# Kernel optimization log

Measured on AMD Instinct MI355X. Metric: run time of the kernel, lower is better.

The kernel has to match this reference:

```python
import jax, jax.numpy as jnp
import numpy as np

HIDDEN = 1024
N_HEADS = 16
HEAD_DIM = 64
LOCAL_WINDOW = 1024
GLOBAL_STRIDE = 512


def _sparse_mask(seq_len):
    # local sliding window (half-window each side), strided global columns, causal
    i = jnp.arange(seq_len)[:, None]
    j = jnp.arange(seq_len)[None, :]
    diff = i - j
    local = jnp.abs(diff) <= (LOCAL_WINDOW // 2)
    glob = (j % GLOBAL_STRIDE) == 0
    causal = diff >= 0
    return (local | glob) & causal  # [S, S] bool


def setup_inputs() -> dict:
    key = jax.random.key(0)
    k0, k1, k2, k3, k4 = jax.random.split(key, 5)
    B, S = 1, 2048
    scale = 1.0 / np.sqrt(HIDDEN)
    return {
        "hidden_states": jax.random.normal(k0, (B, S, HIDDEN), dtype=jnp.float32),
        "w_q": jax.random.normal(k1, (HIDDEN, N_HEADS * HEAD_DIM), dtype=jnp.float32) * scale,
        "w_k": jax.random.normal(k2, (HIDDEN, N_HEADS * HEAD_DIM), dtype=jnp.float32) * scale,
        "w_v": jax.random.normal(k3, (HIDDEN, N_HEADS * HEAD_DIM), dtype=jnp.float32) * scale,
        "w_o": jax.random.normal(k4, (N_HEADS * HEAD_DIM, HIDDEN), dtype=jnp.float32) * scale,
    }


def reference(hidden_states, w_q, w_k, w_v, w_o):
    B, S, _ = hidden_states.shape

    def shape(x):  # [B,S,H*D] -> [B,H,S,D]
        return x.reshape(B, S, N_HEADS, HEAD_DIM).transpose(0, 2, 1, 3)

    q = shape(hidden_states @ w_q)
    k = shape(hidden_states @ w_k)
    v = shape(hidden_states @ w_v)

    scores = jnp.einsum("bhqd,bhkd->bhqk", q, k) / np.sqrt(HEAD_DIM)
    mask = _sparse_mask(S)  # [S,S]
    scores = jnp.where(mask[None, None], scores, -jnp.inf)
    attn = jax.nn.softmax(scores, axis=-1)
    out = jnp.einsum("bhqk,bhkd->bhqd", attn, v)
    out = out.transpose(0, 2, 1, 3).reshape(B, S, N_HEADS * HEAD_DIM)
    return out @ w_o
```

## Files before the change

### kernel.cpp

```cpp
#include <hip/hip_runtime.h>

#define SEQ 2048
#define HID 1024
#define NH 16
#define HD 64
#define QKVLD 3072

typedef __attribute__((ext_vector_type(8))) short bf16x8;
typedef __attribute__((ext_vector_type(4))) float f32x4;

__device__ __forceinline__ unsigned short f2bf(float f) {
  unsigned int x = __float_as_uint(f);
  x += 0x7fffu + ((x >> 16) & 1u);
  return (unsigned short)(x >> 16);
}

__device__ __forceinline__ float bf2f(unsigned short u) {
  return __uint_as_float(((unsigned int)u) << 16);
}

__device__ __forceinline__ void gld_lds16(const void* g, void* l) {
  __builtin_amdgcn_global_load_lds((__attribute__((address_space(1))) void*)g,
                                   (__attribute__((address_space(3))) void*)l, 16, 0, 0);
}

__global__ void prep(const float* __restrict__ X, const float* __restrict__ Wq,
                     const float* __restrict__ Wk, const float* __restrict__ Wv,
                     const float* __restrict__ Wo, unsigned short* __restrict__ Xb,
                     unsigned short* __restrict__ WtQKV, unsigned short* __restrict__ WtO) {
  const int z = blockIdx.z;
  if (z == 4) {
    int bid = blockIdx.y * 32 + blockIdx.x;
    int t = threadIdx.y * 32 + threadIdx.x;
    size_t base = (size_t)bid * 2048 + t * 4;
#pragma unroll
    for (int half = 0; half < 2; half++) {
      float4 v = *(const float4*)(X + base + half * 1024);
      ushort4 o;
      o.x = f2bf(v.x); o.y = f2bf(v.y); o.z = f2bf(v.z); o.w = f2bf(v.w);
      *(ushort4*)(Xb + base + half * 1024) = o;
    }
    return;
  }
  __shared__ float tile[32][33];
  const float* S = (z == 0) ? Wq : (z == 1) ? Wk : (z == 2) ? Wv : Wo;
  unsigned short* D = (z < 3) ? (WtQKV + (size_t)z * HID * HID) : WtO;
  const float scale = (z == 0) ? 0.125f : 1.0f;
  int r0 = blockIdx.y * 32, c0 = blockIdx.x * 32;
  int tx = threadIdx.x, ty = threadIdx.y;
#pragma unroll
  for (int k = 0; k < 4; k++)
    tile[ty + k * 8][tx] = S[(size_t)(r0 + ty + k * 8) * HID + c0 + tx];
  __syncthreads();
#pragma unroll
  for (int k = 0; k < 4; k++)
    D[(size_t)(c0 + ty + k * 8) * HID + r0 + tx] = f2bf(scale * tile[tx][ty + k * 8]);
}

template <int BN, int OUT>
__global__ __launch_bounds__(256, 2) void gemm_bt(const unsigned short* __restrict__ A,
                                                  const unsigned short* __restrict__ Bt,
                                                  void* __restrict__ Cout,
                                                  unsigned short* __restrict__ Vout,
                                                  int M, int N, int K) {
  constexpr int NI = BN / 32;
  __shared__ unsigned short As[128 * 64];
  __shared__ unsigned short Bs[BN * 64];
  const int tid = threadIdx.x;
  const int lane = tid & 63;
  const int w = tid >> 6;
  const int wm = w >> 1, wn = w & 1;
  const int quad = lane >> 4, l16 = lane & 15;
  const int bm = blockIdx.y * 128, bn = blockIdx.x * BN;

  f32x4 acc[4][NI] = {};

  for (int k0 = 0; k0 < K; k0 += 64) {
#pragma unroll
    for (int c = tid; c < 128 * 8; c += 256) {
      int r = c >> 3, kc = c & 7;
      int g = (kc & 4) + ((kc & 3) ^ (r & 3));
      gld_lds16(A + (size_t)(bm + r) * K + k0 + g * 8, As + c * 8);
    }
#pragma unroll
    for (int c = tid; c < BN * 8; c += 256) {
      int r = c >> 3, kc = c & 7;
      int g = (kc & 4) + ((kc & 3) ^ (r & 3));
      gld_lds16(Bt + (size_t)(bn + r) * K + k0 + g * 8, Bs + c * 8);
    }
    __syncthreads();
    bf16x8 af[2][4], bfr[2][NI];
#pragma unroll
    for (int ks = 0; ks < 2; ks++) {
#pragma unroll
      for (int mi = 0; mi < 4; mi++) {
        int m = wm * 64 + mi * 16 + l16;
        af[ks][mi] = *(const bf16x8*)(As + (m * 8 + ks * 4 + (quad ^ (m & 3))) * 8);
      }
#pragma unroll
      for (int ni = 0; ni < NI; ni++) {
        int n = wn * (BN / 2) + ni * 16 + l16;
        bfr[ks][ni] = *(const bf16x8*)(Bs + (n * 8 + ks * 4 + (quad ^ (n & 3))) * 8);
      }
    }
#pragma unroll
    for (int mi = 0; mi < 4; mi++)
#pragma unroll
      for (int ni = 0; ni < NI; ni++) {
        acc[mi][ni] = __builtin_amdgcn_mfma_f32_16x16x32_bf16(af[0][mi], bfr[0][ni], acc[mi][ni], 0, 0, 0);
        acc[mi][ni] = __builtin_amdgcn_mfma_f32_16x16x32_bf16(af[1][mi], bfr[1][ni], acc[mi][ni], 0, 0, 0);
      }
    __syncthreads();
  }

#pragma unroll
  for (int mi = 0; mi < 4; mi++) {
#pragma unroll
    for (int ni = 0; ni < NI; ni++) {
      int row = bm + wm * 64 + mi * 16 + quad * 4;
      int col = bn + wn * (BN / 2) + ni * 16 + l16;
      if (OUT == 0) {
#pragma unroll
        for (int r = 0; r < 4; r++)
          ((float*)Cout)[(size_t)(row + r) * N + col] = acc[mi][ni][r];
      } else {
        if (col < 2 * HID) {
#pragma unroll
          for (int r = 0; r < 4; r++)
            ((unsigned short*)Cout)[(size_t)(row + r) * N + col] = f2bf(acc[mi][ni][r]);
        } else {
          ushort4 o;
          o.x = f2bf(acc[mi][ni][0]); o.y = f2bf(acc[mi][ni][1]);
          o.z = f2bf(acc[mi][ni][2]); o.w = f2bf(acc[mi][ni][3]);
          *(ushort4*)(Vout + (size_t)(col - 2 * HID) * SEQ + row) = o;
        }
      }
    }
  }
}

__global__ __launch_bounds__(256, 2) void attn_sparse(const unsigned short* __restrict__ QKV,
                                                      const unsigned short* __restrict__ VtG,
                                                      unsigned short* __restrict__ AttO) {
  __shared__ unsigned short Ks[64 * 64];
  __shared__ unsigned short Vt[64 * 64];
  __shared__ unsigned short Pw[4][16 * 72];
  const int h = blockIdx.y;
  const int qbase = blockIdx.x * 64;
  const int tid = threadIdx.x;
  const int lane = tid & 63, w = tid >> 6;
  const int quad = lane >> 4, l16 = lane & 15;
  const int qrow0 = qbase + w * 16;
  unsigned short* pws = &Pw[w][0];

  bf16x8 aq[2];
  {
    const unsigned short* qp = QKV + (size_t)(qrow0 + l16) * QKVLD + h * HD + quad * 8;
    aq[0] = *(const bf16x8*)qp;
    aq[1] = *(const bf16x8*)(qp + 32);
  }

  f32x4 accO[4] = {};
  float lsum = 0.f;

  const int jlo = (qbase >= 512) ? (qbase - 512) : 0;
  const int ng = (jlo > 0) ? ((jlo + 511) >> 9) : 0;
  const int ntl = ((qbase - jlo) >> 6) + 1;

  for (int t = 0; t < ntl; t++) {
    const int j0 = jlo + t * 64;
    if (t > 0) __syncthreads();
#pragma unroll
    for (int c = tid; c < 512; c += 256) {
      int r = c >> 3, kc = c & 7;
      int g = (kc & 4) + ((kc & 3) ^ (r & 3));
      gld_lds16(QKV + (size_t)(j0 + r) * QKVLD + HID + h * HD + g * 8, Ks + c * 8);
      gld_lds16(VtG + (size_t)(h * HD + r) * SEQ + j0 + g * 8, Vt + c * 8);
    }
    __syncthreads();

    f32x4 s[4] = {};
#pragma unroll
    for (int nj = 0; nj < 4; nj++) {
      int row = nj * 16 + l16;
#pragma unroll
      for (int ks = 0; ks < 2; ks++) {
        bf16x8 ak = *(const bf16x8*)(Ks + (row * 8 + ks * 4 + (quad ^ (row & 3))) * 8);
        s[nj] = __builtin_amdgcn_mfma_f32_16x16x32_bf16(ak, aq[ks], s[nj], 0, 0, 0);
      }
    }

    const bool isdiag = (t == ntl - 1);
    const bool istrail = (t == 0) && (qbase >= 512);
    const int trailg = (istrail && ((j0 & 511) == 0)) ? 1 : 0;
    const int db = qrow0 + l16 - j0 - quad * 4;
#pragma unroll
    for (int nj = 0; nj < 4; nj++) {
      float p[4];
#pragma unroll
      for (int r = 0; r < 4; r++) {
        float x = fminf(s[nj][r], 60.0f);
        int d = db - nj * 16 - r;
        bool valid = true;
        if (isdiag) valid = (d >= 0);
        else if (istrail) valid = (d <= 512) || (trailg && (nj * 16 + quad * 4 + r) == 0);
        x = valid ? x : -1e30f;
        p[r] = __expf(x);
        lsum += p[r];
      }
      unsigned int u01 = (unsigned)f2bf(p[0]) | ((unsigned)f2bf(p[1]) << 16);
      unsigned int u23 = (unsigned)f2bf(p[2]) | ((unsigned)f2bf(p[3]) << 16);
      *(uint2*)(pws + l16 * 72 + nj * 16 + quad * 4) = make_uint2(u01, u23);
    }

#pragma unroll
    for (int kk = 0; kk < 2; kk++) {
      bf16x8 bp = *(const bf16x8*)(pws + l16 * 72 + kk * 32 + quad * 8);
#pragma unroll
      for (int nd = 0; nd < 4; nd++) {
        int row = nd * 16 + l16;
        bf16x8 av = *(const bf16x8*)(Vt + (row * 8 + kk * 4 + (quad ^ (row & 3))) * 8);
        accO[nd] = __builtin_amdgcn_mfma_f32_16x16x32_bf16(av, bp, accO[nd], 0, 0, 0);
      }
    }
  }

  if (ng > 0) {
    __syncthreads();
    if (tid < ng * 8) {
      int r = tid >> 3, kc = tid & 7;
      int g = (kc & 4) + ((kc & 3) ^ (r & 3));
      *(uint4*)(Ks + tid * 8) =
          *(const uint4*)(QKV + ((size_t)r << 9) * QKVLD + HID + h * HD + g * 8);
    }
    if (tid < ng * 64) {
      int d = tid & 63, c = tid >> 6;
      Vt[(d * 8 + (d & 3)) * 8 + c] = VtG[(size_t)(h * HD + d) * SEQ + ((size_t)c << 9)];
    }
    __syncthreads();
    f32x4 s0 = {};
#pragma unroll
    for (int ks = 0; ks < 2; ks++) {
      bf16x8 ak = *(const bf16x8*)(Ks + (l16 * 8 + ks * 4 + (quad ^ (l16 & 3))) * 8);
      s0 = __builtin_amdgcn_mfma_f32_16x16x32_bf16(ak, aq[ks], s0, 0, 0, 0);
    }
    float p[4];
#pragma unroll
    for (int r = 0; r < 4; r++) {
      p[r] = ((quad * 4 + r) < ng) ? __expf(fminf(s0[r], 60.0f)) : 0.f;
      lsum += p[r];
    }
    unsigned int u01 = (unsigned)f2bf(p[0]) | ((unsigned)f2bf(p[1]) << 16);
    unsigned int u23 = (unsigned)f2bf(p[2]) | ((unsigned)f2bf(p[3]) << 16);
    *(uint2*)(pws + l16 * 72 + quad * 4) = make_uint2(u01, u23);
    *(uint2*)(pws + l16 * 72 + 16 + quad * 4) = make_uint2(0, 0);
    bf16x8 bp = *(const bf16x8*)(pws + l16 * 72 + quad * 8);
#pragma unroll
    for (int nd = 0; nd < 4; nd++) {
      int row = nd * 16 + l16;
      bf16x8 av = *(const bf16x8*)(Vt + (row * 8 + (quad ^ (row & 3))) * 8);
      accO[nd] = __builtin_amdgcn_mfma_f32_16x16x32_bf16(av, bp, accO[nd], 0, 0, 0);
    }
  }

  lsum += __shfl_xor(lsum, 16);
  lsum += __shfl_xor(lsum, 32);
  const float rl = 1.0f / lsum;
  const int i = qrow0 + l16;
#pragma unroll
  for (int nd = 0; nd < 4; nd++) {
    ushort4 o;
    o.x = f2bf(accO[nd][0] * rl);
    o.y = f2bf(accO[nd][1] * rl);
    o.z = f2bf(accO[nd][2] * rl);
    o.w = f2bf(accO[nd][3] * rl);
    *(ushort4*)(AttO + (size_t)i * HID + h * HD + nd * 16 + quad * 4) = o;
  }
}

extern "C" void kernel_launch(void* const* d_in, const int* in_sizes, int n_in,
                              void* d_out, int out_size, void* d_ws, size_t ws_size,
                              hipStream_t stream) {
  const float* X  = (const float*)d_in[0];
  const float* Wq = (const float*)d_in[1];
  const float* Wk = (const float*)d_in[2];
  const float* Wv = (const float*)d_in[3];
  const float* Wo = (const float*)d_in[4];
  float* out = (float*)d_out;

  unsigned short* Xb    = (unsigned short*)d_ws;
  unsigned short* WtQKV = Xb + (size_t)SEQ * HID;
  unsigned short* WtO   = WtQKV + (size_t)QKVLD * HID;
  unsigned short* QKV   = WtO + (size_t)HID * HID;
  unsigned short* VtG   = QKV + (size_t)SEQ * QKVLD;
  unsigned short* AttO  = VtG + (size_t)HID * SEQ;

  prep<<<dim3(32, 32, 5), dim3(32, 8), 0, stream>>>(X, Wq, Wk, Wv, Wo, Xb, WtQKV, WtO);

  gemm_bt<96, 2><<<dim3(QKVLD / 96, SEQ / 128), dim3(256), 0, stream>>>(
      Xb, WtQKV, QKV, VtG, SEQ, QKVLD, HID);

  attn_sparse<<<dim3(SEQ / 64, NH), dim3(256), 0, stream>>>(QKV, VtG, AttO);

  gemm_bt<64, 0><<<dim3(HID / 64, SEQ / 128), dim3(256), 0, stream>>>(
      AttO, WtO, out, nullptr, SEQ, HID, HID);
}
```

Measured before the change: 133.1 us.

## Fuse all stages into one persistent kernel with grid barriers and XCD-aware tiling

Replaces the four separate launches (prep, QKV GEMM, sparse attention, output GEMM) with one persistent 512-block kernel. Stages are separated by software grid barriers built on atomics. Block-to-tile mappings are remapped by XCD index to improve L2 locality. The output GEMM uses 64x64 tiles, bf16 packing uses the hardware paired conversion, and the fminf clamp before exp is removed. This trades launch gaps and stage tails for barrier spin cost and a risk of deadlock if all 512 blocks are not co-resident.

```diff
diff --git a/kernel.cpp b/kernel.cpp
--- a/kernel.cpp
+++ b/kernel.cpp
@@ -1,4 +1,5 @@
 #include <hip/hip_runtime.h>
+#include <hip/hip_bf16.h>
 
 #define SEQ 2048
 #define HID 1024
@@ -8,15 +9,18 @@
 
 typedef __attribute__((ext_vector_type(8))) short bf16x8;
 typedef __attribute__((ext_vector_type(4))) float f32x4;
-
-__device__ __forceinline__ unsigned short f2bf(float f) {
+typedef unsigned short us;
+
+__device__ __forceinline__ us f2bf(float f) {
   unsigned int x = __float_as_uint(f);
   x += 0x7fffu + ((x >> 16) & 1u);
-  return (unsigned short)(x >> 16);
-}
-
-__device__ __forceinline__ float bf2f(unsigned short u) {
-  return __uint_as_float(((unsigned int)u) << 16);
+  return (us)(x >> 16);
+}
+
+__device__ __forceinline__ unsigned int pkbf(float a, float b) {
+  union { __hip_bfloat162 h2; unsigned int u; } cvt;
+  cvt.h2 = __float22bfloat162_rn(make_float2(a, b));
+  return cvt.u;
 }
 
 __device__ __forceinline__ void gld_lds16(const void* g, void* l) {
@@ -24,257 +28,323 @@
                                    (__attribute__((address_space(3))) void*)l, 16, 0, 0);
 }
 
-__global__ void prep(const float* __restrict__ X, const float* __restrict__ Wq,
-                     const float* __restrict__ Wk, const float* __restrict__ Wv,
-                     const float* __restrict__ Wo, unsigned short* __restrict__ Xb,
-                     unsigned short* __restrict__ WtQKV, unsigned short* __restrict__ WtO) {
-  const int z = blockIdx.z;
-  if (z == 4) {
-    int bid = blockIdx.y * 32 + blockIdx.x;
-    int t = threadIdx.y * 32 + threadIdx.x;
-    size_t base = (size_t)bid * 2048 + t * 4;
-#pragma unroll
-    for (int half = 0; half < 2; half++) {
-      float4 v = *(const float4*)(X + base + half * 1024);
-      ushort4 o;
-      o.x = f2bf(v.x); o.y = f2bf(v.y); o.z = f2bf(v.z); o.w = f2bf(v.w);
-      *(ushort4*)(Xb + base + half * 1024) = o;
-    }
-    return;
-  }
-  __shared__ float tile[32][33];
-  const float* S = (z == 0) ? Wq : (z == 1) ? Wk : (z == 2) ? Wv : Wo;
-  unsigned short* D = (z < 3) ? (WtQKV + (size_t)z * HID * HID) : WtO;
-  const float scale = (z == 0) ? 0.125f : 1.0f;
-  int r0 = blockIdx.y * 32, c0 = blockIdx.x * 32;
-  int tx = threadIdx.x, ty = threadIdx.y;
-#pragma unroll
-  for (int k = 0; k < 4; k++)
-    tile[ty + k * 8][tx] = S[(size_t)(r0 + ty + k * 8) * HID + c0 + tx];
+__device__ __forceinline__ f32x4 mfma(bf16x8 a, bf16x8 b, f32x4 c) {
+  return __builtin_amdgcn_mfma_f32_16x16x32_bf16(a, b, c, 0, 0, 0);
+}
+
+#define NBLK 512
+
+__device__ __forceinline__ void gridbar(unsigned int* bar, int idx) {
   __syncthreads();
-#pragma unroll
-  for (int k = 0; k < 4; k++)
-    D[(size_t)(c0 + ty + k * 8) * HID + r0 + tx] = f2bf(scale * tile[tx][ty + k * 8]);
-}
-
-template <int BN, int OUT>
-__global__ __launch_bounds__(256, 2) void gemm_bt(const unsigned short* __restrict__ A,
-                                                  const unsigned short* __restrict__ Bt,
-                                                  void* __restrict__ Cout,
-                                                  unsigned short* __restrict__ Vout,
-                                                  int M, int N, int K) {
-  constexpr int NI = BN / 32;
-  __shared__ unsigned short As[128 * 64];
-  __shared__ unsigned short Bs[BN * 64];
-  const int tid = threadIdx.x;
-  const int lane = tid & 63;
-  const int w = tid >> 6;
-  const int wm = w >> 1, wn = w & 1;
-  const int quad = lane >> 4, l16 = lane & 15;
-  const int bm = blockIdx.y * 128, bn = blockIdx.x * BN;
-
-  f32x4 acc[4][NI] = {};
-
-  for (int k0 = 0; k0 < K; k0 += 64) {
-#pragma unroll
-    for (int c = tid; c < 128 * 8; c += 256) {
-      int r = c >> 3, kc = c & 7;
-      int g = (kc & 4) + ((kc & 3) ^ (r & 3));
-      gld_lds16(A + (size_t)(bm + r) * K + k0 + g * 8, As + c * 8);
-    }
-#pragma unroll
-    for (int c = tid; c < BN * 8; c += 256) {
-      int r = c >> 3, kc = c & 7;
-      int g = (kc & 4) + ((kc & 3) ^ (r & 3));
-      gld_lds16(Bt + (size_t)(bn + r) * K + k0 + g * 8, Bs + c * 8);
-    }
-    __syncthreads();
-    bf16x8 af[2][4], bfr[2][NI];
-#pragma unroll
-    for (int ks = 0; ks < 2; ks++) {
-#pragma unroll
-      for (int mi = 0; mi < 4; mi++) {
-        int m = wm * 64 + mi * 16 + l16;
-        af[ks][mi] = *(const bf16x8*)(As + (m * 8 + ks * 4 + (quad ^ (m & 3))) * 8);
-      }
-#pragma unroll
-      for (int ni = 0; ni < NI; ni++) {
-        int n = wn * (BN / 2) + ni * 16 + l16;
-        bfr[ks][ni] = *(const bf16x8*)(Bs + (n * 8 + ks * 4 + (quad ^ (n & 3))) * 8);
-      }
-    }
-#pragma unroll
-    for (int mi = 0; mi < 4; mi++)
-#pragma unroll
-      for (int ni = 0; ni < NI; ni++) {
-        acc[mi][ni] = __builtin_amdgcn_mfma_f32_16x16x32_bf16(af[0][mi], bfr[0][ni], acc[mi][ni], 0, 0, 0);
-        acc[mi][ni] = __builtin_amdgcn_mfma_f32_16x16x32_bf16(af[1][mi], bfr[1][ni], acc[mi][ni], 0, 0, 0);
-      }
-    __syncthreads();
-  }
-
-#pragma unroll
-  for (int mi = 0; mi < 4; mi++) {
-#pragma unroll
-    for (int ni = 0; ni < NI; ni++) {
-      int row = bm + wm * 64 + mi * 16 + quad * 4;
-      int col = bn + wn * (BN / 2) + ni * 16 + l16;
-      if (OUT == 0) {
-#pragma unroll
-        for (int r = 0; r < 4; r++)
-          ((float*)Cout)[(size_t)(row + r) * N + col] = acc[mi][ni][r];
-      } else {
-        if (col < 2 * HID) {
-#pragma unroll
-          for (int r = 0; r < 4; r++)
-            ((unsigned short*)Cout)[(size_t)(row + r) * N + col] = f2bf(acc[mi][ni][r]);
-        } else {
-          ushort4 o;
-          o.x = f2bf(acc[mi][ni][0]); o.y = f2bf(acc[mi][ni][1]);
-          o.z = f2bf(acc[mi][ni][2]); o.w = f2bf(acc[mi][ni][3]);
-          *(ushort4*)(Vout + (size_t)(col - 2 * HID) * SEQ + row) = o;
-        }
-      }
-    }
-  }
-}
-
-__global__ __launch_bounds__(256, 2) void attn_sparse(const unsigned short* __restrict__ QKV,
-                                                      const unsigned short* __restrict__ VtG,
-                                                      unsigned short* __restrict__ AttO) {
-  __shared__ unsigned short Ks[64 * 64];
-  __shared__ unsigned short Vt[64 * 64];
-  __shared__ unsigned short Pw[4][16 * 72];
-  const int h = blockIdx.y;
-  const int qbase = blockIdx.x * 64;
+  if (threadIdx.x == 0) {
+    __threadfence();
+    unsigned int prev = atomicAdd(&bar[idx * 2], 1u);
+    if (prev == NBLK - 1) {
+      atomicExch(&bar[idx * 2 + 1], 1u);
+    } else {
+      while (atomicAdd(&bar[idx * 2 + 1], 0u) == 0u)
+        __builtin_amdgcn_s_sleep(8);
+    }
+    __threadfence();
+  }
+  __syncthreads();
+}
+
+__global__ void bar_init(unsigned int* bar) {
+  if (threadIdx.x < 8) bar[threadIdx.x] = 0u;
+}
+
+__global__ __launch_bounds__(256, 2) void fused(
+    const float* __restrict__ X, const float* __restrict__ Wq,
+    const float* __restrict__ Wk, const float* __restrict__ Wv,
+    const float* __restrict__ Wo, float* __restrict__ out,
+    us* __restrict__ Xb, us* __restrict__ WtQKV, us* __restrict__ WtO,
+    us* __restrict__ QKV, us* __restrict__ VtG, us* __restrict__ AttO,
+    unsigned int* bar) {
+  __shared__ __align__(16) unsigned char smem[28672];
+  const int lin = blockIdx.x;
   const int tid = threadIdx.x;
   const int lane = tid & 63, w = tid >> 6;
   const int quad = lane >> 4, l16 = lane & 15;
-  const int qrow0 = qbase + w * 16;
-  unsigned short* pws = &Pw[w][0];
-
-  bf16x8 aq[2];
+
   {
-    const unsigned short* qp = QKV + (size_t)(qrow0 + l16) * QKVLD + h * HD + quad * 8;
-    aq[0] = *(const bf16x8*)qp;
-    aq[1] = *(const bf16x8*)(qp + 32);
-  }
-
-  f32x4 accO[4] = {};
-  float lsum = 0.f;
-
-  const int jlo = (qbase >= 512) ? (qbase - 512) : 0;
-  const int ng = (jlo > 0) ? ((jlo + 511) >> 9) : 0;
-  const int ntl = ((qbase - jlo) >> 6) + 1;
-
-  for (int t = 0; t < ntl; t++) {
-    const int j0 = jlo + t * 64;
-    if (t > 0) __syncthreads();
-#pragma unroll
-    for (int c = tid; c < 512; c += 256) {
-      int r = c >> 3, kc = c & 7;
-      int g = (kc & 4) + ((kc & 3) ^ (r & 3));
-      gld_lds16(QKV + (size_t)(j0 + r) * QKVLD + HID + h * HD + g * 8, Ks + c * 8);
-      gld_lds16(VtG + (size_t)(h * HD + r) * SEQ + j0 + g * 8, Vt + c * 8);
-    }
-    __syncthreads();
-
-    f32x4 s[4] = {};
-#pragma unroll
-    for (int nj = 0; nj < 4; nj++) {
-      int row = nj * 16 + l16;
+    size_t base = (size_t)lin * 4096 + tid * 4;
+#pragma unroll
+    for (int i = 0; i < 4; i++) {
+      float4 v = *(const float4*)(X + base + i * 1024);
+      *(uint2*)(Xb + base + i * 1024) = make_uint2(pkbf(v.x, v.y), pkbf(v.z, v.w));
+    }
+    float* tile = (float*)smem;
+    const int tx = tid & 31, ty = tid >> 5;
+    for (int tt = lin; tt < 4096; tt += 512) {
+      const int z = tt >> 10, rem = tt & 1023;
+      const int r0 = (rem >> 5) * 32, c0 = (rem & 31) * 32;
+      const float* S = (z == 0) ? Wq : (z == 1) ? Wk : (z == 2) ? Wv : Wo;
+      us* D = (z < 3) ? (WtQKV + (size_t)z * HID * HID) : WtO;
+      const float scale = (z == 0) ? 0.125f : 1.0f;
+#pragma unroll
+      for (int k = 0; k < 4; k++)
+        tile[(ty + k * 8) * 33 + tx] = S[(size_t)(r0 + ty + k * 8) * HID + c0 + tx];
+      __syncthreads();
+#pragma unroll
+      for (int k = 0; k < 4; k++)
+        D[(size_t)(c0 + ty + k * 8) * HID + r0 + tx] = f2bf(scale * tile[tx * 33 + ty + k * 8]);
+      __syncthreads();
+    }
+  }
+  gridbar(bar, 0);
+
+  {
+    us* As = (us*)smem;
+    us* Bs = As + 128 * 64;
+    const int wm = w >> 1, wn = w & 1;
+    const int xcd = lin & 7, idx = lin >> 3;
+    const int bx = (xcd & 3) * 8 + (idx & 7);
+    const int by = (xcd >> 2) * 8 + (idx >> 3);
+    const int bm = by * 128, bn = bx * 96;
+
+    f32x4 acc[4][3] = {};
+
+    for (int k0 = 0; k0 < HID; k0 += 64) {
+#pragma unroll
+      for (int c = tid; c < 1024; c += 256) {
+        int r = c >> 3, kc = c & 7;
+        int g = (kc & 4) + ((kc & 3) ^ (r & 3));
+        gld_lds16(Xb + (size_t)(bm + r) * HID + k0 + g * 8, As + c * 8);
+      }
+#pragma unroll
+      for (int c = tid; c < 768; c += 256) {
+        int r = c >> 3, kc = c & 7;
+        int g = (kc & 4) + ((kc & 3) ^ (r & 3));
+        gld_lds16(WtQKV + (size_t)(bn + r) * HID + k0 + g * 8, Bs + c * 8);
+      }
+      __syncthreads();
+      bf16x8 af[2][4], bfr[2][3];
 #pragma unroll
       for (int ks = 0; ks < 2; ks++) {
-        bf16x8 ak = *(const bf16x8*)(Ks + (row * 8 + ks * 4 + (quad ^ (row & 3))) * 8);
-        s[nj] = __builtin_amdgcn_mfma_f32_16x16x32_bf16(ak, aq[ks], s[nj], 0, 0, 0);
-      }
-    }
-
-    const bool isdiag = (t == ntl - 1);
-    const bool istrail = (t == 0) && (qbase >= 512);
-    const int trailg = (istrail && ((j0 & 511) == 0)) ? 1 : 0;
-    const int db = qrow0 + l16 - j0 - quad * 4;
-#pragma unroll
-    for (int nj = 0; nj < 4; nj++) {
+#pragma unroll
+        for (int mi = 0; mi < 4; mi++) {
+          int m = wm * 64 + mi * 16 + l16;
+          af[ks][mi] = *(const bf16x8*)(As + (m * 8 + ks * 4 + (quad ^ (m & 3))) * 8);
+        }
+#pragma unroll
+        for (int ni = 0; ni < 3; ni++) {
+          int n = wn * 48 + ni * 16 + l16;
+          bfr[ks][ni] = *(const bf16x8*)(Bs + (n * 8 + ks * 4 + (quad ^ (n & 3))) * 8);
+        }
+      }
+#pragma unroll
+      for (int mi = 0; mi < 4; mi++)
+#pragma unroll
+        for (int ni = 0; ni < 3; ni++) {
+          acc[mi][ni] = mfma(af[0][mi], bfr[0][ni], acc[mi][ni]);
+          acc[mi][ni] = mfma(af[1][mi], bfr[1][ni], acc[mi][ni]);
+        }
+      __syncthreads();
+    }
+
+#pragma unroll
+    for (int mi = 0; mi < 4; mi++) {
+#pragma unroll
+      for (int ni = 0; ni < 3; ni++) {
+        int row = bm + wm * 64 + mi * 16 + quad * 4;
+        int col = bn + wn * 48 + ni * 16 + l16;
+        if (col < 2 * HID) {
+#pragma unroll
+          for (int r = 0; r < 4; r++)
+            QKV[(size_t)(row + r) * QKVLD + col] = f2bf(acc[mi][ni][r]);
+        } else {
+          *(uint2*)(VtG + (size_t)(col - 2 * HID) * SEQ + row) =
+              make_uint2(pkbf(acc[mi][ni][0], acc[mi][ni][1]),
+                         pkbf(acc[mi][ni][2], acc[mi][ni][3]));
+        }
+      }
+    }
+  }
+  gridbar(bar, 1);
+
+  {
+    us* Ks = (us*)smem;
+    us* Vt = Ks + 4096;
+    us* Pw = Vt + 4096;
+    const int xcd = lin & 7, slot = lin >> 3;
+    const int h = slot >> 2;
+    const int qbase = (xcd * 4 + (slot & 3)) * 64;
+    const int qrow0 = qbase + w * 16;
+    us* pws = Pw + w * (16 * 72);
+
+    bf16x8 aq[2];
+    {
+      const us* qp = QKV + (size_t)(qrow0 + l16) * QKVLD + h * HD + quad * 8;
+      aq[0] = *(const bf16x8*)qp;
+      aq[1] = *(const bf16x8*)(qp + 32);
+    }
+
+    f32x4 accO[4] = {};
+    float lsum = 0.f;
+
+    const int jlo = (qbase >= 512) ? (qbase - 512) : 0;
+    const int ng = (jlo > 0) ? ((jlo + 511) >> 9) : 0;
+    const int ntl = ((qbase - jlo) >> 6) + 1;
+
+    for (int t = 0; t < ntl; t++) {
+      const int j0 = jlo + t * 64;
+      if (t > 0) __syncthreads();
+#pragma unroll
+      for (int c = tid; c < 512; c += 256) {
+        int r = c >> 3, kc = c & 7;
+        int g = (kc & 4) + ((kc & 3) ^ (r & 3));
+        gld_lds16(QKV + (size_t)(j0 + r) * QKVLD + HID + h * HD + g * 8, Ks + c * 8);
+        gld_lds16(VtG + (size_t)(h * HD + r) * SEQ + j0 + g * 8, Vt + c * 8);
+      }
+      __syncthreads();
+
+      f32x4 s[4] = {};
+#pragma unroll
+      for (int nj = 0; nj < 4; nj++) {
+        int row = nj * 16 + l16;
+#pragma unroll
+        for (int ks = 0; ks < 2; ks++) {
+          bf16x8 ak = *(const bf16x8*)(Ks + (row * 8 + ks * 4 + (quad ^ (row & 3))) * 8);
+          s[nj] = mfma(ak, aq[ks], s[nj]);
+        }
+      }
+
+      const bool isdiag = (t == ntl - 1);
+      const bool istrail = (t == 0) && (qbase >= 512);
+      const int trailg = (istrail && ((j0 & 511) == 0)) ? 1 : 0;
+      const int db = qrow0 + l16 - j0 - quad * 4;
+#pragma unroll
+      for (int nj = 0; nj < 4; nj++) {
+        float p[4];
+#pragma unroll
+        for (int r = 0; r < 4; r++) {
+          float x = s[nj][r];
+          int d = db - nj * 16 - r;
+          bool valid = true;
+          if (isdiag) valid = (d >= 0);
+          else if (istrail) valid = (d <= 512) || (trailg && (nj * 16 + quad * 4 + r) == 0);
+          x = valid ? x : -1e30f;
+          p[r] = __expf(x);
+          lsum += p[r];
+        }
+        *(uint2*)(pws + l16 * 72 + nj * 16 + quad * 4) =
+            make_uint2(pkbf(p[0], p[1]), pkbf(p[2], p[3]));
+      }
+
+#pragma unroll
+      for (int kk = 0; kk < 2; kk++) {
+        bf16x8 bp = *(const bf16x8*)(pws + l16 * 72 + kk * 32 + quad * 8);
+#pragma unroll
+        for (int nd = 0; nd < 4; nd++) {
+          int row = nd * 16 + l16;
+          bf16x8 av = *(const bf16x8*)(Vt + (row * 8 + kk * 4 + (quad ^ (row & 3))) * 8);
+          accO[nd] = mfma(av, bp, accO[nd]);
+        }
+      }
+    }
+
+    if (ng > 0) {
+      __syncthreads();
+      if (tid < ng * 8) {
+        int r = tid >> 3, kc = tid & 7;
+        int g = (kc & 4) + ((kc & 3) ^ (r & 3));
+        *(uint4*)(Ks + tid * 8) =
+            *(const uint4*)(QKV + ((size_t)r << 9) * QKVLD + HID + h * HD + g * 8);
+      }
+      if (tid < ng * 64) {
+        int d = tid & 63, c = tid >> 6;
+        Vt[(d * 8 + (d & 3)) * 8 + c] = VtG[(size_t)(h * HD + d) * SEQ + ((size_t)c << 9)];
+      }
+      __syncthreads();
+      f32x4 s0 = {};
+#pragma unroll
+      for (int ks = 0; ks < 2; ks++) {
+        bf16x8 ak = *(const bf16x8*)(Ks + (l16 * 8 + ks * 4 + (quad ^ (l16 & 3))) * 8);
+        s0 = mfma(ak, aq[ks], s0);
+      }
       float p[4];
 #pragma unroll
       for (int r = 0; r < 4; r++) {
-        float x = fminf(s[nj][r], 60.0f);
-        int d = db - nj * 16 - r;
-        bool valid = true;
-        if (isdiag) valid = (d >= 0);
-        else if (istrail) valid = (d <= 512) || (trailg && (nj * 16 + quad * 4 + r) == 0);
-        x = valid ? x : -1e30f;
-        p[r] = __expf(x);
+        p[r] = ((quad * 4 + r) < ng) ? __expf(s0[r]) : 0.f;
         lsum += p[r];
       }
-      unsigned int u01 = (unsigned)f2bf(p[0]) | ((unsigned)f2bf(p[1]) << 16);
-      unsigned int u23 = (unsigned)f2bf(p[2]) | ((unsigned)f2bf(p[3]) << 16);
-      *(uint2*)(pws + l16 * 72 + nj * 16 + quad * 4) = make_uint2(u01, u23);
-    }
-
-#pragma unroll
-    for (int kk = 0; kk < 2; kk++) {
-      bf16x8 bp = *(const bf16x8*)(pws + l16 * 72 + kk * 32 + quad * 8);
+      *(uint2*)(pws + l16 * 72 + quad * 4) = make_uint2(pkbf(p[0], p[1]), pkbf(p[2], p[3]));
+      *(uint2*)(pws + l16 * 72 + 16 + quad * 4) = make_uint2(0, 0);
+      bf16x8 bp = *(const bf16x8*)(pws + l16 * 72 + quad * 8);
 #pragma unroll
       for (int nd = 0; nd < 4; nd++) {
         int row = nd * 16 + l16;
-        bf16x8 av = *(const bf16x8*)(Vt + (row * 8 + kk * 4 + (quad ^ (row & 3))) * 8);
-        accO[nd] = __builtin_amdgcn_mfma_f32_16x16x32_bf16(av, bp, accO[nd], 0, 0, 0);
-      }
-    }
-  }
-
-  if (ng > 0) {
-    __syncthreads();
-    if (tid < ng * 8) {
-      int r = tid >> 3, kc = tid & 7;
-      int g = (kc & 4) + ((kc & 3) ^ (r & 3));
-      *(uint4*)(Ks + tid * 8) =
-          *(const uint4*)(QKV + ((size_t)r << 9) * QKVLD + HID + h * HD + g * 8);
-    }
-    if (tid < ng * 64) {
-      int d = tid & 63, c = tid >> 6;
-      Vt[(d * 8 + (d & 3)) * 8 + c] = VtG[(size_t)(h * HD + d) * SEQ + ((size_t)c << 9)];
-    }
-    __syncthreads();
-    f32x4 s0 = {};
-#pragma unroll
-    for (int ks = 0; ks < 2; ks++) {
-      bf16x8 ak = *(const bf16x8*)(Ks + (l16 * 8 + ks * 4 + (quad ^ (l16 & 3))) * 8);
-      s0 = __builtin_amdgcn_mfma_f32_16x16x32_bf16(ak, aq[ks], s0, 0, 0, 0);
-    }
-    float p[4];
-#pragma unroll
-    for (int r = 0; r < 4; r++) {
-      p[r] = ((quad * 4 + r) < ng) ? __expf(fminf(s0[r], 60.0f)) : 0.f;
-      lsum += p[r];
-    }
-    unsigned int u01 = (unsigned)f2bf(p[0]) | ((unsigned)f2bf(p[1]) << 16);
-    unsigned int u23 = (unsigned)f2bf(p[2]) | ((unsigned)f2bf(p[3]) << 16);
-    *(uint2*)(pws + l16 * 72 + quad * 4) = make_uint2(u01, u23);
-    *(uint2*)(pws + l16 * 72 + 16 + quad * 4) = make_uint2(0, 0);
-    bf16x8 bp = *(const bf16x8*)(pws + l16 * 72 + quad * 8);
+        bf16x8 av = *(const bf16x8*)(Vt + (row * 8 + (quad ^ (row & 3))) * 8);
+        accO[nd] = mfma(av, bp, accO[nd]);
+      }
+    }
+
+    lsum += __shfl_xor(lsum, 16);
+    lsum += __shfl_xor(lsum, 32);
+    const float rl = 1.0f / lsum;
+    const int i = qrow0 + l16;
 #pragma unroll
     for (int nd = 0; nd < 4; nd++) {
-      int row = nd * 16 + l16;
-      bf16x8 av = *(const bf16x8*)(Vt + (row * 8 + (quad ^ (row & 3))) * 8);
-      accO[nd] = __builtin_amdgcn_mfma_f32_16x16x32_bf16(av, bp, accO[nd], 0, 0, 0);
-    }
-  }
-
-  lsum += __shfl_xor(lsum, 16);
-  lsum += __shfl_xor(lsum, 32);
-  const float rl = 1.0f / lsum;
-  const int i = qrow0 + l16;
-#pragma unroll
-  for (int nd = 0; nd < 4; nd++) {
-    ushort4 o;
-    o.x = f2bf(accO[nd][0] * rl);
-    o.y = f2bf(accO[nd][1] * rl);
-    o.z = f2bf(accO[nd][2] * rl);
-    o.w = f2bf(accO[nd][3] * rl);
-    *(ushort4*)(AttO + (size_t)i * HID + h * HD + nd * 16 + quad * 4) = o;
+      *(uint2*)(AttO + (size_t)i * HID + h * HD + nd * 16 + quad * 4) =
+          make_uint2(pkbf(accO[nd][0] * rl, accO[nd][1] * rl),
+                     pkbf(accO[nd][2] * rl, accO[nd][3] * rl));
+    }
+  }
+  gridbar(bar, 2);
+
+  {
+    us* As = (us*)smem;
+    us* Bs = As + 64 * 64;
+    const int wm = w >> 1, wn = w & 1;
+    const int xcd = lin & 7, idx = lin >> 3;
+    const int bx = (xcd & 3) * 4 + (idx & 3);
+    const int by = (xcd >> 2) * 16 + (idx >> 2);
+    const int bm = by * 64, bn = bx * 64;
+
+    f32x4 acc[2][2] = {};
+
+    for (int k0 = 0; k0 < HID; k0 += 64) {
+#pragma unroll
+      for (int c = tid; c < 512; c += 256) {
+        int r = c >> 3, kc = c & 7;
+        int g = (kc & 4) + ((kc & 3) ^ (r & 3));
+        gld_lds16(AttO + (size_t)(bm + r) * HID + k0 + g * 8, As + c * 8);
+        gld_lds16(WtO + (size_t)(bn + r) * HID + k0 + g * 8, Bs + c * 8);
+      }
+      __syncthreads();
+#pragma unroll
+      for (int ks = 0; ks < 2; ks++) {
+        bf16x8 af[2], bfr[2];
+#pragma unroll
+        for (int mi = 0; mi < 2; mi++) {
+          int m = wm * 32 + mi * 16 + l16;
+          af[mi] = *(const bf16x8*)(As + (m * 8 + ks * 4 + (quad ^ (m & 3))) * 8);
+        }
+#pragma unroll
+        for (int ni = 0; ni < 2; ni++) {
+          int n = wn * 32 + ni * 16 + l16;
+          bfr[ni] = *(const bf16x8*)(Bs + (n * 8 + ks * 4 + (quad ^ (n & 3))) * 8);
+        }
+#pragma unroll
+        for (int mi = 0; mi < 2; mi++)
+#pragma unroll
+          for (int ni = 0; ni < 2; ni++)
+            acc[mi][ni] = mfma(af[mi], bfr[ni], acc[mi][ni]);
+      }
+      __syncthreads();
+    }
+
+#pragma unroll
+    for (int mi = 0; mi < 2; mi++)
+#pragma unroll
+      for (int ni = 0; ni < 2; ni++) {
+        int row = bm + wm * 32 + mi * 16 + quad * 4;
+        int col = bn + wn * 32 + ni * 16 + l16;
+#pragma unroll
+        for (int r = 0; r < 4; r++)
+          out[(size_t)(row + r) * HID + col] = acc[mi][ni][r];
+      }
   }
 }
 
@@ -288,20 +358,15 @@
   const float* Wo = (const float*)d_in[4];
   float* out = (float*)d_out;
 
-  unsigned short* Xb    = (unsigned short*)d_ws;
-  unsigned short* WtQKV = Xb + (size_t)SEQ * HID;
-  unsigned short* WtO   = WtQKV + (size_t)QKVLD * HID;
-  unsigned short* QKV   = WtO + (size_t)HID * HID;
-  unsigned short* VtG   = QKV + (size_t)SEQ * QKVLD;
-  unsigned short* AttO  = VtG + (size_t)HID * SEQ;
-
-  prep<<<dim3(32, 32, 5), dim3(32, 8), 0, stream>>>(X, Wq, Wk, Wv, Wo, Xb, WtQKV, WtO);
-
-  gemm_bt<96, 2><<<dim3(QKVLD / 96, SEQ / 128), dim3(256), 0, stream>>>(
-      Xb, WtQKV, QKV, VtG, SEQ, QKVLD, HID);
-
-  attn_sparse<<<dim3(SEQ / 64, NH), dim3(256), 0, stream>>>(QKV, VtG, AttO);
-
-  gemm_bt<64, 0><<<dim3(HID / 64, SEQ / 128), dim3(256), 0, stream>>>(
-      AttO, WtO, out, nullptr, SEQ, HID, HID);
-}
+  us* Xb    = (us*)d_ws;
+  us* WtQKV = Xb + (size_t)SEQ * HID;
+  us* WtO   = WtQKV + (size_t)QKVLD * HID;
+  us* QKV   = WtO + (size_t)HID * HID;
+  us* VtG   = QKV + (size_t)SEQ * QKVLD;
+  us* AttO  = VtG + (size_t)HID * SEQ;
+  unsigned int* bar = (unsigned int*)((char*)d_ws + (64u << 20));
+
+  bar_init<<<dim3(1), dim3(64), 0, stream>>>(bar);
+  fused<<<dim3(NBLK), dim3(256), 0, stream>>>(X, Wq, Wk, Wv, Wo, out,
+                                              Xb, WtQKV, WtO, QKV, VtG, AttO, bar);
+}
```

Result: slower. 272.6 us (+104.8%).
